# Kernel tuning notes

Measured on AMD Instinct MI355X. Metric: run time of the kernel, lower is better.

The kernel has to match this reference:

```python
import jax, jax.numpy as jnp
import numpy as np

S, N, D = 65536, 8192, 128  # images, texts, embed dim


def setup_inputs() -> dict:
    key = jax.random.key(0)
    k1, k2, k3 = jax.random.split(key, 3)
    return {
        "image_features": jax.random.normal(k1, (S, D), dtype=jnp.float32),
        "text_features": jax.random.normal(k2, (N, D), dtype=jnp.float32),
        "key": jax.random.randint(k3, (S,), 0, N),
        "logit_scale": jnp.asarray(10.0, dtype=jnp.float32),  # already exponentiated temperature
        "logit_bias": jnp.asarray(-10.0, dtype=jnp.float32),
    }


def _l2norm(x):
    return x / (jnp.linalg.norm(x, ord=2, axis=-1, keepdims=True) + 1e-12)


def reference(image_features, text_features, key, logit_scale, logit_bias):
    s = image_features.shape[0]
    n = text_features.shape[0]
    zimg = _l2norm(image_features)           # (s, d)
    ztxt = _l2norm(text_features)            # (n, d)

    # True-positive logits: only the diagonal gather of the full (s, n) matmul is used,
    # so compute it directly as a row-wise dot product.
    tp_logits = jnp.einsum("sd,sd->s", zimg, ztxt[key]) * logit_scale + logit_bias
    pot_losses = jax.nn.softplus(-tp_logits)  # (s,)

    # Segmented argmin over images grouped by their text key (pick_best_candidate=True).
    seg_min = jax.ops.segment_min(pot_losses, key, num_segments=n)        # (n,)
    counts = jax.ops.segment_sum(jnp.ones((s,), jnp.int32), key, num_segments=n)
    valid = counts > 0                                                    # (n,)
    is_min = pot_losses == seg_min[key]
    cand_idx = jnp.where(is_min, jnp.arange(s), s)                        # first-occurrence tie-break
    best = jax.ops.segment_min(cand_idx, key, num_segments=n)             # (n,)
    best = jnp.where(valid, best, 0)

    zimg_sel = jnp.where(valid[:, None], zimg[best], 0.0)                 # (n, d)

    logits = zimg_sel @ ztxt.T * logit_scale + logit_bias                 # (n, n)
    diag = jnp.eye(n, dtype=bool)
    # labels*logits == logits on diagonal, -logits off-diagonal; softplus(-labels*logits):
    terms = jax.nn.softplus(jnp.where(diag, -logits, logits))
    mask = valid[:, None] & valid[None, :]
    num_valid = jnp.sum(valid)
    loss = jnp.sum(jnp.where(mask, terms, 0.0)) / jnp.maximum(num_valid, 1).astype(terms.dtype)
    return loss
```

## Files before the change

### kernel.cpp

```cpp
#include <hip/hip_runtime.h>
#include <stdint.h>

#define D 128

typedef __attribute__((ext_vector_type(4))) float float4v;
typedef long long frag8;

__device__ __forceinline__ float hw_exp2(float x) { return __builtin_amdgcn_exp2f(x); }
__device__ __forceinline__ float hw_log2(float x) { return __builtin_amdgcn_logf(x); }

__device__ __forceinline__ float softplus_fast(float x) {
    float e = hw_exp2(x * 1.44269504f);
    return 0.69314718f * hw_log2(1.0f + e);
}

__device__ __forceinline__ unsigned short f2fp8x2(float x, float y) {
    int p = __builtin_amdgcn_cvt_pk_fp8_f32(x, y, 0, false);
    return (unsigned short)(p & 0xFFFF);
}

__device__ __forceinline__ float dot4(float4 a, float4 b) {
    return a.x * b.x + a.y * b.y + a.z * b.z + a.w * b.w;
}

__global__ __launch_bounds__(256) void k_ztxt(const float* __restrict__ txt,
                                              float* __restrict__ tinv,
                                              uint8_t* __restrict__ ztxt_f8,
                                              unsigned long long* __restrict__ packed,
                                              double* __restrict__ partial) {
    int wave = threadIdx.x >> 6;
    int lane = threadIdx.x & 63;
    int n = blockIdx.x * 4 + wave;
    if (blockIdx.x == 0) partial[threadIdx.x] = 0.0;
    if (lane == 0) packed[n] = ~0ull;
    const float2 v = *(const float2*)(txt + (size_t)n * D + lane * 2);
    float ss = v.x * v.x + v.y * v.y;
    #pragma unroll
    for (int off = 32; off; off >>= 1) ss += __shfl_xor(ss, off);
    float inv = 1.0f / (sqrtf(ss) + 1e-12f);
    if (lane == 0) tinv[n] = inv;
    *(unsigned short*)(ztxt_f8 + (size_t)n * D + lane * 2) =
        f2fp8x2(v.x * inv, v.y * inv);
}

__global__ __launch_bounds__(256) void k_tp(const float* __restrict__ img,
                                            const float* __restrict__ txt,
                                            const float* __restrict__ tinv,
                                            const int* __restrict__ key,
                                            const float* __restrict__ sc,
                                            const float* __restrict__ bi,
                                            unsigned long long* __restrict__ packed,
                                            int S) {
    int t = threadIdx.x;
    int grp = t >> 4, gl = t & 15;
    int s = blockIdx.x * 16 + grp;
    if (s >= S) return;
    int k = key[s];
    const float4* ia = (const float4*)(img + (size_t)s * D);
    const float4* tb = (const float4*)(txt + (size_t)k * D);
    float4 a0 = ia[gl], a1 = ia[16 + gl];
    float4 b0 = tb[gl], b1 = tb[16 + gl];
    float ss = dot4(a0, a0) + dot4(a1, a1);
    float dt = dot4(a0, b0) + dot4(a1, b1);
    #pragma unroll
    for (int off = 8; off; off >>= 1) {
        ss += __shfl_xor(ss, off);
        dt += __shfl_xor(dt, off);
    }
    if (gl == 0) {
        float inv = 1.0f / (sqrtf(ss) + 1e-12f);
        float tp = dt * inv * tinv[k] * (*sc) + (*bi);
        float pot = softplus_fast(-tp);
        unsigned long long p =
            ((unsigned long long)__float_as_uint(pot) << 32) | (unsigned int)s;
        atomicMin(&packed[k], p);
    }
}

__global__ __launch_bounds__(256) void k_select(const float* __restrict__ img,
                                               const unsigned long long* __restrict__ packed,
                                               uint8_t* __restrict__ zsel_f8,
                                               float* __restrict__ validF) {
    int wave = threadIdx.x >> 6;
    int lane = threadIdx.x & 63;
    int n = blockIdx.x * 4 + wave;
    unsigned long long p = packed[n];
    bool valid = (p != ~0ull);
    if (!valid) {
        if (lane == 0) validF[n] = 0.0f;
        *(unsigned short*)(zsel_f8 + (size_t)n * D + lane * 2) = 0;
        return;
    }
    int s = (int)(unsigned int)(p & 0xFFFFFFFFull);
    const float2 a = *(const float2*)(img + (size_t)s * D + lane * 2);
    float ss = a.x * a.x + a.y * a.y;
    #pragma unroll
    for (int off = 32; off; off >>= 1) ss += __shfl_xor(ss, off);
    float inv = 1.0f / (sqrtf(ss) + 1e-12f);
    *(unsigned short*)(zsel_f8 + (size_t)n * D + lane * 2) =
        f2fp8x2(a.x * inv, a.y * inv);
    if (lane == 0) validF[n] = 1.0f;
}

__global__ __launch_bounds__(512, 4) void k_gemm(const uint8_t* __restrict__ A,
                                                 const uint8_t* __restrict__ B,
                                                 const float* __restrict__ validF,
                                                 const float* __restrict__ sc,
                                                 const float* __restrict__ bi,
                                                 double* __restrict__ partial) {
    __shared__ __align__(16) uint8_t As[256 * 136];
    __shared__ __align__(16) uint8_t Bs[128 * 136];
    __shared__ float vI[256];
    __shared__ float vJ[128];
    __shared__ float wsum[8];

    const int t = threadIdx.x;
    const int i0 = blockIdx.y * 256;
    const int j0 = blockIdx.x * 128;

    if (t < 256) vI[t] = validF[i0 + t];
    else if (t < 384) vJ[t - 256] = validF[j0 + t - 256];

    const int wave = t >> 6, lane = t & 63;
    const int wm = (wave >> 1) * 64;
    const int wn = (wave & 1) * 64;
    const int lr = lane & 15;
    const int kq = (lane >> 4) * 8;

    {
        const int rowA = t >> 1, colA = (t & 1) * 64;
        const uint8_t* ga = A + (size_t)(i0 + rowA) * D + colA;
        uint8_t* la = As + rowA * 136 + colA;
        ulonglong2 a0 = *(const ulonglong2*)(ga);
        ulonglong2 a1 = *(const ulonglong2*)(ga + 16);
        ulonglong2 a2 = *(const ulonglong2*)(ga + 32);
        ulonglong2 a3 = *(const ulonglong2*)(ga + 48);
        *(unsigned long long*)(la)      = a0.x;
        *(unsigned long long*)(la + 8)  = a0.y;
        *(unsigned long long*)(la + 16) = a1.x;
        *(unsigned long long*)(la + 24) = a1.y;
        *(unsigned long long*)(la + 32) = a2.x;
        *(unsigned long long*)(la + 40) = a2.y;
        *(unsigned long long*)(la + 48) = a3.x;
        *(unsigned long long*)(la + 56) = a3.y;
        const int rowB = t >> 2, colB = (t & 3) * 32;
        const uint8_t* gb = B + (size_t)(j0 + rowB) * D + colB;
        uint8_t* lb = Bs + rowB * 136 + colB;
        ulonglong2 b0 = *(const ulonglong2*)(gb);
        ulonglong2 b1 = *(const ulonglong2*)(gb + 16);
        *(unsigned long long*)(lb)      = b0.x;
        *(unsigned long long*)(lb + 8)  = b0.y;
        *(unsigned long long*)(lb + 16) = b1.x;
        *(unsigned long long*)(lb + 24) = b1.y;
    }
    __syncthreads();

    float4v acc[4][4];
    #pragma unroll
    for (int mi = 0; mi < 4; ++mi)
        #pragma unroll
        for (int ni = 0; ni < 4; ++ni)
            acc[mi][ni] = (float4v){0.f, 0.f, 0.f, 0.f};

    #pragma unroll
    for (int k0 = 0; k0 < 128; k0 += 32) {
        frag8 bf[4];
        #pragma unroll
        for (int ni = 0; ni < 4; ++ni)
            bf[ni] = *(const frag8*)(Bs + (wn + ni * 16 + lr) * 136 + k0 + kq);
        #pragma unroll
        for (int mi = 0; mi < 4; ++mi) {
            frag8 af = *(const frag8*)(As + (wm + mi * 16 + lr) * 136 + k0 + kq);
            #pragma unroll
            for (int ni = 0; ni < 4; ++ni)
                acc[mi][ni] = __builtin_amdgcn_mfma_f32_16x16x32_fp8_fp8(
                    af, bf[ni], acc[mi][ni], 0, 0, 0);
        }
    }

    const float scale = *sc, bias = *bi;
    const float sl = scale * 1.44269504f, bl = bias * 1.44269504f;
    const int rb = (lane >> 4) * 4;
    float vjv[4], viv[4][4];
    #pragma unroll
    for (int ni = 0; ni < 4; ++ni) vjv[ni] = vJ[wn + ni * 16 + lr];
    #pragma unroll
    for (int mi = 0; mi < 4; ++mi)
        #pragma unroll
        for (int r = 0; r < 4; ++r) viv[mi][r] = vI[wm + mi * 16 + rb + r];

    float sum = 0.0f;
    if ((blockIdx.x >> 1) != blockIdx.y) {
        #pragma unroll
        for (int ni = 0; ni < 4; ++ni) {
            float s = 0.0f;
            #pragma unroll
            for (int mi = 0; mi < 4; ++mi)
                #pragma unroll
                for (int r = 0; r < 4; ++r) {
                    float u = hw_exp2(fmaf(acc[mi][ni][r], sl, bl));
                    s = fmaf(u, viv[mi][r], s);
                }
            sum = fmaf(s, vjv[ni], sum);
        }
    } else {
        const int dof = j0 - i0;
        #pragma unroll
        for (int ni = 0; ni < 4; ++ni) {
            float s = 0.0f;
            const int lj = wn + ni * 16 + lr;
            #pragma unroll
            for (int mi = 0; mi < 4; ++mi)
                #pragma unroll
                for (int r = 0; r < 4; ++r) {
                    const int li = wm + mi * 16 + rb + r;
                    float l = fmaf(acc[mi][ni][r], scale, bias);
                    float u = hw_exp2(-fabsf(l) * 1.44269504f);
                    float g = fmaxf(l, 0.0f) + fmaf(-0.5f * u, u, u);
                    if (li == lj + dof) g -= l;
                    s = fmaf(g, viv[mi][r], s);
                }
            sum = fmaf(s, vjv[ni], sum);
        }
    }
    #pragma unroll
    for (int off = 32; off; off >>= 1) sum += __shfl_xor(sum, off);
    if (lane == 0) wsum[wave] = sum;
    __syncthreads();
    if (t == 0) {
        float bs = 0.f;
        #pragma unroll
        for (int w = 0; w < 8; ++w) bs += wsum[w];
        atomicAdd(&partial[(blockIdx.y * 64 + blockIdx.x) & 255], (double)bs);
    }
}

__global__ __launch_bounds__(256) void k_final(const double* __restrict__ partial,
                                               const float* __restrict__ validF,
                                               float* __restrict__ out, int N) {
    __shared__ float wsum[4];
    __shared__ double dsum[4];
    int wave = threadIdx.x >> 6, lane = threadIdx.x & 63;
    float s = 0.0f;
    for (int i = threadIdx.x; i < N; i += 256) s += validF[i];
    double d = partial[threadIdx.x];
    #pragma unroll
    for (int off = 32; off; off >>= 1) {
        s += __shfl_xor(s, off);
        d += __shfl_xor(d, off);
    }
    if (lane == 0) { wsum[wave] = s; dsum[wave] = d; }
    __syncthreads();
    if (threadIdx.x == 0) {
        float nv = wsum[0] + wsum[1] + wsum[2] + wsum[3];
        if (nv < 1.0f) nv = 1.0f;
        double tot = dsum[0] + dsum[1] + dsum[2] + dsum[3];
        out[0] = (float)(tot / (double)nv);
    }
}

extern "C" void kernel_launch(void* const* d_in, const int* in_sizes, int n_in,
                              void* d_out, int out_size, void* d_ws, size_t ws_size,
                              hipStream_t stream) {
    const float* img = (const float*)d_in[0];
    const float* txt = (const float*)d_in[1];
    const int*   key = (const int*)d_in[2];
    const float* sc  = (const float*)d_in[3];
    const float* bi  = (const float*)d_in[4];
    float* out = (float*)d_out;

    const int S = in_sizes[2];
    const int N = in_sizes[1] / D;

    char* ws = (char*)d_ws;
    size_t off = 0;
    auto carve = [&](size_t bytes) {
        void* p = ws + off;
        off = (off + bytes + 255) & ~(size_t)255;
        return p;
    };
    float*              tinv    = (float*)carve((size_t)N * sizeof(float));
    uint8_t*            ztxt_f8 = (uint8_t*)carve((size_t)N * D);
    uint8_t*            zsel_f8 = (uint8_t*)carve((size_t)N * D);
    unsigned long long* packed  = (unsigned long long*)carve((size_t)N * sizeof(unsigned long long));
    float*              validF  = (float*)carve((size_t)N * sizeof(float));
    double*             partial = (double*)carve(256 * sizeof(double));

    k_ztxt<<<N / 4, 256, 0, stream>>>(txt, tinv, ztxt_f8, packed, partial);
    k_tp<<<(S + 15) / 16, 256, 0, stream>>>(img, txt, tinv, key, sc, bi, packed, S);
    k_select<<<N / 4, 256, 0, stream>>>(img, packed, zsel_f8, validF);
    dim3 g(N / 128, N / 256);
    k_gemm<<<g, 512, 0, stream>>>(zsel_f8, ztxt_f8, validF, sc, bi, partial);
    k_final<<<1, 256, 0, stream>>>(partial, validF, out, N);
}
```

Baseline: 114.9 us.

## Fuse prep kernels, merge final reduce into GEMM, swizzled direct-to-LDS loads

Merges the text-normalise and true-positive kernels into one launch, recomputing the text norm inline so tinv no longer needs to be stored. The packed buffer is now initialised with a memset, and the final reduction moves into the GEMM through a last-block counter, which removes a launch. GEMM tile loads switch to global_load_lds with an XOR swizzle in place of padded LDS rows. The intent is to cut launch overhead and LDS staging cost, at the price of an extra memset and added synchronisation complexity.

Measured after the change: 139.8 us. 1.22x slower.

```diff
diff --git a/kernel.cpp b/kernel.cpp
--- a/kernel.cpp
+++ b/kernel.cpp
@@ -23,66 +23,75 @@
     return a.x * b.x + a.y * b.y + a.z * b.z + a.w * b.w;
 }
 
-__global__ __launch_bounds__(256) void k_ztxt(const float* __restrict__ txt,
-                                              float* __restrict__ tinv,
+__device__ __forceinline__ void gload_lds16(const uint8_t* g, uint8_t* l) {
+    __builtin_amdgcn_global_load_lds(
+        (const __attribute__((address_space(1))) void*)g,
+        (__attribute__((address_space(3))) void*)l, 16, 0, 0);
+}
+
+__global__ __launch_bounds__(256) void k_prep(const float* __restrict__ img,
+                                              const float* __restrict__ txt,
+                                              const int* __restrict__ key,
+                                              const float* __restrict__ sc,
+                                              const float* __restrict__ bi,
                                               uint8_t* __restrict__ ztxt_f8,
                                               unsigned long long* __restrict__ packed,
-                                              double* __restrict__ partial) {
-    int wave = threadIdx.x >> 6;
-    int lane = threadIdx.x & 63;
-    int n = blockIdx.x * 4 + wave;
-    if (blockIdx.x == 0) partial[threadIdx.x] = 0.0;
-    if (lane == 0) packed[n] = ~0ull;
-    const float2 v = *(const float2*)(txt + (size_t)n * D + lane * 2);
-    float ss = v.x * v.x + v.y * v.y;
-    #pragma unroll
-    for (int off = 32; off; off >>= 1) ss += __shfl_xor(ss, off);
-    float inv = 1.0f / (sqrtf(ss) + 1e-12f);
-    if (lane == 0) tinv[n] = inv;
-    *(unsigned short*)(ztxt_f8 + (size_t)n * D + lane * 2) =
-        f2fp8x2(v.x * inv, v.y * inv);
-}
-
-__global__ __launch_bounds__(256) void k_tp(const float* __restrict__ img,
-                                            const float* __restrict__ txt,
-                                            const float* __restrict__ tinv,
-                                            const int* __restrict__ key,
-                                            const float* __restrict__ sc,
-                                            const float* __restrict__ bi,
-                                            unsigned long long* __restrict__ packed,
-                                            int S) {
-    int t = threadIdx.x;
-    int grp = t >> 4, gl = t & 15;
-    int s = blockIdx.x * 16 + grp;
-    if (s >= S) return;
-    int k = key[s];
-    const float4* ia = (const float4*)(img + (size_t)s * D);
-    const float4* tb = (const float4*)(txt + (size_t)k * D);
-    float4 a0 = ia[gl], a1 = ia[16 + gl];
-    float4 b0 = tb[gl], b1 = tb[16 + gl];
-    float ss = dot4(a0, a0) + dot4(a1, a1);
-    float dt = dot4(a0, b0) + dot4(a1, b1);
-    #pragma unroll
-    for (int off = 8; off; off >>= 1) {
-        ss += __shfl_xor(ss, off);
-        dt += __shfl_xor(dt, off);
-    }
-    if (gl == 0) {
+                                              int nPack, int S) {
+    const int t = threadIdx.x;
+    if ((int)blockIdx.x < nPack) {
+        int wave = t >> 6, lane = t & 63;
+        int n = blockIdx.x * 4 + wave;
+        const float2 v = *(const float2*)(txt + (size_t)n * D + lane * 2);
+        float ss = v.x * v.x + v.y * v.y;
+        #pragma unroll
+        for (int off = 32; off; off >>= 1) ss += __shfl_xor(ss, off);
         float inv = 1.0f / (sqrtf(ss) + 1e-12f);
-        float tp = dt * inv * tinv[k] * (*sc) + (*bi);
-        float pot = softplus_fast(-tp);
-        unsigned long long p =
-            ((unsigned long long)__float_as_uint(pot) << 32) | (unsigned int)s;
-        atomicMin(&packed[k], p);
+        *(unsigned short*)(ztxt_f8 + (size_t)n * D + lane * 2) =
+            f2fp8x2(v.x * inv, v.y * inv);
+    } else {
+        int grp = t >> 4, gl = t & 15;
+        int s = ((int)blockIdx.x - nPack) * 16 + grp;
+        if (s < S) {
+            int k = key[s];
+            const float4* ia = (const float4*)(img + (size_t)s * D);
+            const float4* tb = (const float4*)(txt + (size_t)k * D);
+            float4 a0 = ia[gl], a1 = ia[16 + gl];
+            float4 b0 = tb[gl], b1 = tb[16 + gl];
+            float ss = dot4(a0, a0) + dot4(a1, a1);
+            float dt = dot4(a0, b0) + dot4(a1, b1);
+            float tt = dot4(b0, b0) + dot4(b1, b1);
+            #pragma unroll
+            for (int off = 8; off; off >>= 1) {
+                ss += __shfl_xor(ss, off);
+                dt += __shfl_xor(dt, off);
+                tt += __shfl_xor(tt, off);
+            }
+            if (gl == 0) {
+                float inv_i = 1.0f / (sqrtf(ss) + 1e-12f);
+                float inv_t = 1.0f / (sqrtf(tt) + 1e-12f);
+                float tp = dt * inv_i * inv_t * (*sc) + (*bi);
+                float pot = softplus_fast(-tp);
+                unsigned long long p =
+                    ((unsigned long long)__float_as_uint(pot) << 32) | (unsigned int)s;
+                atomicMin(&packed[k], p);
+            }
+        }
     }
 }
 
 __global__ __launch_bounds__(256) void k_select(const float* __restrict__ img,
                                                const unsigned long long* __restrict__ packed,
                                                uint8_t* __restrict__ zsel_f8,
-                                               float* __restrict__ validF) {
-    int wave = threadIdx.x >> 6;
-    int lane = threadIdx.x & 63;
+                                               float* __restrict__ validF,
+                                               double* __restrict__ partial,
+                                               unsigned int* __restrict__ counter) {
+    int t = threadIdx.x;
+    if (blockIdx.x == 0) {
+        partial[t] = 0.0;
+        if (t == 0) *counter = 0u;
+    }
+    int wave = t >> 6;
+    int lane = t & 63;
     int n = blockIdx.x * 4 + wave;
     unsigned long long p = packed[n];
     bool valid = (p != ~0ull);
@@ -107,12 +116,17 @@
                                                  const float* __restrict__ validF,
                                                  const float* __restrict__ sc,
                                                  const float* __restrict__ bi,
-                                                 double* __restrict__ partial) {
-    __shared__ __align__(16) uint8_t As[256 * 136];
-    __shared__ __align__(16) uint8_t Bs[128 * 136];
+                                                 double* __restrict__ partial,
+                                                 unsigned int* __restrict__ counter,
+                                                 float* __restrict__ out, int N) {
+    __shared__ __align__(16) uint8_t As[256 * 128];
+    __shared__ __align__(16) uint8_t Bs[128 * 128];
     __shared__ float vI[256];
     __shared__ float vJ[128];
     __shared__ float wsum[8];
+    __shared__ float fred[8];
+    __shared__ double dred[8];
+    __shared__ int lastB;
 
     const int t = threadIdx.x;
     const int i0 = blockIdx.y * 256;
@@ -126,32 +140,23 @@
     const int wn = (wave & 1) * 64;
     const int lr = lane & 15;
     const int kq = (lane >> 4) * 8;
+    const int swz = (lr & 7) << 4;
 
     {
-        const int rowA = t >> 1, colA = (t & 1) * 64;
-        const uint8_t* ga = A + (size_t)(i0 + rowA) * D + colA;
-        uint8_t* la = As + rowA * 136 + colA;
-        ulonglong2 a0 = *(const ulonglong2*)(ga);
-        ulonglong2 a1 = *(const ulonglong2*)(ga + 16);
-        ulonglong2 a2 = *(const ulonglong2*)(ga + 32);
-        ulonglong2 a3 = *(const ulonglong2*)(ga + 48);
-        *(unsigned long long*)(la)      = a0.x;
-        *(unsigned long long*)(la + 8)  = a0.y;
-        *(unsigned long long*)(la + 16) = a1.x;
-        *(unsigned long long*)(la + 24) = a1.y;
-        *(unsigned long long*)(la + 32) = a2.x;
-        *(unsigned long long*)(la + 40) = a2.y;
-        *(unsigned long long*)(la + 48) = a3.x;
-        *(unsigned long long*)(la + 56) = a3.y;
-        const int rowB = t >> 2, colB = (t & 3) * 32;
-        const uint8_t* gb = B + (size_t)(j0 + rowB) * D + colB;
-        uint8_t* lb = Bs + rowB * 136 + colB;
-        ulonglong2 b0 = *(const ulonglong2*)(gb);
-        ulonglong2 b1 = *(const ulonglong2*)(gb + 16);
-        *(unsigned long long*)(lb)      = b0.x;
-        *(unsigned long long*)(lb + 8)  = b0.y;
-        *(unsigned long long*)(lb + 16) = b1.x;
-        *(unsigned long long*)(lb + 24) = b1.y;
+        const uint8_t* gA = A + (size_t)i0 * D;
+        const uint8_t* gB = B + (size_t)j0 * D;
+        #pragma unroll
+        for (int j = 0; j < 4; ++j) {
+            int L = wave * 4096 + j * 1024 + lane * 16;
+            int src = (L & ~127) | ((((L >> 4) ^ (L >> 7)) & 7) << 4);
+            gload_lds16(gA + src, As + wave * 4096 + j * 1024);
+        }
+        #pragma unroll
+        for (int j = 0; j < 2; ++j) {
+            int L = wave * 2048 + j * 1024 + lane * 16;
+            int src = (L & ~127) | ((((L >> 4) ^ (L >> 7)) & 7) << 4);
+            gload_lds16(gB + src, Bs + wave * 2048 + j * 1024);
+        }
     }
     __syncthreads();
 
@@ -167,10 +172,10 @@
         frag8 bf[4];
         #pragma unroll
         for (int ni = 0; ni < 4; ++ni)
-            bf[ni] = *(const frag8*)(Bs + (wn + ni * 16 + lr) * 136 + k0 + kq);
+            bf[ni] = *(const frag8*)(Bs + (wn + ni * 16 + lr) * 128 + ((k0 + kq) ^ swz));
         #pragma unroll
         for (int mi = 0; mi < 4; ++mi) {
-            frag8 af = *(const frag8*)(As + (wm + mi * 16 + lr) * 136 + k0 + kq);
+            frag8 af = *(const frag8*)(As + (wm + mi * 16 + lr) * 128 + ((k0 + kq) ^ swz));
             #pragma unroll
             for (int ni = 0; ni < 4; ++ni)
                 acc[mi][ni] = __builtin_amdgcn_mfma_f32_16x16x32_fp8_fp8(
@@ -231,31 +236,30 @@
         float bs = 0.f;
         #pragma unroll
         for (int w = 0; w < 8; ++w) bs += wsum[w];
-        atomicAdd(&partial[(blockIdx.y * 64 + blockIdx.x) & 255], (double)bs);
-    }
-}
-
-__global__ __launch_bounds__(256) void k_final(const double* __restrict__ partial,
-                                               const float* __restrict__ validF,
-                                               float* __restrict__ out, int N) {
-    __shared__ float wsum[4];
-    __shared__ double dsum[4];
-    int wave = threadIdx.x >> 6, lane = threadIdx.x & 63;
-    float s = 0.0f;
-    for (int i = threadIdx.x; i < N; i += 256) s += validF[i];
-    double d = partial[threadIdx.x];
-    #pragma unroll
-    for (int off = 32; off; off >>= 1) {
-        s += __shfl_xor(s, off);
-        d += __shfl_xor(d, off);
-    }
-    if (lane == 0) { wsum[wave] = s; dsum[wave] = d; }
+        atomicAdd(&partial[(blockIdx.y * gridDim.x + blockIdx.x) & 255], (double)bs);
+        __threadfence();
+        unsigned int v = atomicAdd(counter, 1u);
+        lastB = (v == gridDim.x * gridDim.y - 1u);
+    }
     __syncthreads();
-    if (threadIdx.x == 0) {
-        float nv = wsum[0] + wsum[1] + wsum[2] + wsum[3];
-        if (nv < 1.0f) nv = 1.0f;
-        double tot = dsum[0] + dsum[1] + dsum[2] + dsum[3];
-        out[0] = (float)(tot / (double)nv);
+    if (lastB) {
+        float nv = 0.f;
+        for (int i = t; i < N; i += 512) nv += validF[i];
+        double ds = (t < 256) ? atomicAdd(&partial[t], 0.0) : 0.0;
+        #pragma unroll
+        for (int off = 32; off; off >>= 1) {
+            nv += __shfl_xor(nv, off);
+            ds += __shfl_xor(ds, off);
+        }
+        if (lane == 0) { fred[wave] = nv; dred[wave] = ds; }
+        __syncthreads();
+        if (t == 0) {
+            float nvt = 0.f; double tot = 0.0;
+            #pragma unroll
+            for (int w = 0; w < 8; ++w) { nvt += fred[w]; tot += dred[w]; }
+            if (nvt < 1.0f) nvt = 1.0f;
+            out[0] = (float)(tot / (double)nvt);
+        }
     }
 }
 
@@ -279,17 +283,19 @@
         off = (off + bytes + 255) & ~(size_t)255;
         return p;
     };
-    float*              tinv    = (float*)carve((size_t)N * sizeof(float));
     uint8_t*            ztxt_f8 = (uint8_t*)carve((size_t)N * D);
     uint8_t*            zsel_f8 = (uint8_t*)carve((size_t)N * D);
     unsigned long long* packed  = (unsigned long long*)carve((size_t)N * sizeof(unsigned long long));
     float*              validF  = (float*)carve((size_t)N * sizeof(float));
     double*             partial = (double*)carve(256 * sizeof(double));
-
-    k_ztxt<<<N / 4, 256, 0, stream>>>(txt, tinv, ztxt_f8, packed, partial);
-    k_tp<<<(S + 15) / 16, 256, 0, stream>>>(img, txt, tinv, key, sc, bi, packed, S);
-    k_select<<<N / 4, 256, 0, stream>>>(img, packed, zsel_f8, validF);
+    unsigned int*       counter = (unsigned int*)carve(sizeof(unsigned int));
+
+    hipMemsetAsync(packed, 0xFF, (size_t)N * sizeof(unsigned long long), stream);
+
+    const int nPack = N / 4;
+    k_prep<<<nPack + (S + 15) / 16, 256, 0, stream>>>(img, txt, key, sc, bi,
+                                                      ztxt_f8, packed, nPack, S);
+    k_select<<<N / 4, 256, 0, stream>>>(img, packed, zsel_f8, validF, partial, counter);
     dim3 g(N / 128, N / 256);
-    k_gemm<<<g, 512, 0, stream>>>(zsel_f8, ztxt_f8, validF, sc, bi, partial);
-    k_final<<<1, 256, 0, stream>>>(partial, validF, out, N);
-}
+    k_gemm<<<g, 512, 0, stream>>>(zsel_f8, ztxt_f8, validF, sc, bi, partial, counter, out, N);
+}
```
